# Optimization experiments

Measured on AMD Instinct MI355X. Metric: run time of the kernel, lower is better.

## Reference

```python
import jax, jax.numpy as jnp
import numpy as np

# ---- constants mirroring the torch module ----
LOSS_ALPHA = 1.0      # args.loss_weight_alpha (intra-class weight)
LOSS_BETA = 1.0       # args.loss_weight_beta (focal weight)
FOCAL_GAMMA = 2.0
FOCAL_ALPHA = 0.85
EPS = 1e-09
LDAM_S = 30.0
CLS_NUM = np.array([85.0, 900.0])
LDAM_MAX_M = 0.5
LDAM_W = np.array([0.15, 0.85], dtype=np.float32)
B = 16777216


def setup_inputs() -> dict:
    key = jax.random.key(0)
    k1, k2 = jax.random.split(key)
    x = jax.random.uniform(k1, (B, 2), dtype=jnp.float32)  # [B, 2] probabilities-like logits
    target = jax.random.randint(k2, (B,), 0, 2)            # binary labels
    return {"x": x, "target": target}


def _intraclass_p(centered, std, target, cls):
    # correlation between consecutive same-class rows (sorted-index order),
    # vectorized: class-c indices first via stable argsort, mask invalid pairs.
    n_rows = centered.shape[0]
    mask = target == cls
    n = jnp.sum(mask)
    order = jnp.argsort(jnp.where(mask, jnp.arange(n_rows), n_rows))
    a, b = order[:-1], order[1:]
    corr = jnp.sum(centered[a] * centered[b], axis=1) / (std[a] * std[b])
    valid = jnp.arange(n_rows - 1) < (n - 1)
    s = jnp.sum(jnp.where(valid, corr, 0.0))
    return jnp.where(n > 0, s / jnp.maximum(n, 1).astype(s.dtype), 0.0)


def reference(x, target):
    num_cls = x.shape[1]
    # ---- LDAM loss ----
    m = 1.0 / np.sqrt(np.sqrt(CLS_NUM))
    m = m * (LDAM_MAX_M / np.max(m))
    m_list = jnp.asarray(m, jnp.float32)
    w = jnp.asarray(LDAM_W)
    batch_m = m_list[target]                                      # [B]
    onehot = jax.nn.one_hot(target, num_cls, dtype=bool)          # [B, C]
    out = jnp.where(onehot, x - batch_m[:, None], x)              # margin on target logit only
    logsm = jax.nn.log_softmax(LDAM_S * out, axis=-1)
    nll = -jnp.take_along_axis(logsm, target[:, None], axis=1)[:, 0]
    wi = w[target]
    ldam = jnp.sum(wi * nll) / jnp.sum(wi)                        # weighted-mean cross entropy
    # ---- binary focal loss (treats x[:,1] as probability) ----
    p = x[:, 1]
    t = target.astype(x.dtype)
    fl = (-FOCAL_ALPHA * t * (1.0 - p) ** FOCAL_GAMMA * jnp.log(p + EPS)
          - (1.0 - FOCAL_ALPHA) * (1.0 - t) * p ** FOCAL_GAMMA * jnp.log(1.0 - p + EPS))
    focal = jnp.mean(fl)
    # ---- intra-class correlation loss ----
    centered = x - jnp.mean(x, axis=1, keepdims=True)
    std = jnp.std(x, axis=1, ddof=1)                               # torch.std default: unbiased
    p0 = _intraclass_p(centered, std, target, 0)
    p1 = _intraclass_p(centered, std, target, 1)
    intra = (p0 - p1) ** 2
    return ldam + LOSS_BETA * focal + LOSS_ALPHA * intra
```

## Files before the change

### kernel.cpp

```cpp
#include <hip/hip_runtime.h>

#define E_BLOCK 1024

#define M1f     0.2771814156f
#define C_A1    60.0f
#define C_C1    (30.0f*M1f - 15.0f)

#define EXP2F(v) __builtin_amdgcn_exp2f(v)
#define LOG2F(v) __builtin_amdgcn_logf(v)

__device__ __forceinline__ void comb0(int &s, int &f, int &l, int sb, int fb, int lb) {
  s += sb + l * fb;
  f = f ? f : fb;
  l = fb ? lb : l;
}

__device__ __forceinline__ void bfly_step(int m, int lane, int &s, int &f, int &l) {
  const int os = __shfl_xor(s, m), of = __shfl_xor(f, m), ol = __shfl_xor(l, m);
  const bool up = (lane & m) != 0;
  int as = up ? os : s, af = up ? of : f, al = up ? ol : l;
  const int bs = up ? s : os, bf = up ? f : of, bl = up ? l : ol;
  comb0(as, af, al, bs, bf, bl);
  s = as; f = af; l = al;
}

__device__ __forceinline__ void elem_all(float x0, float x1, int t,
    float &wnll, float &flraw, int &cnt1,
    int &s0, int &f0, int &l0, int &s1, int &f1, int &l1) {
  const float tf  = (float)t;
  const float wgt = fmaf(tf, 0.7f, 0.15f);
  const float d   = x0 - x1;
  const float za  = fmaf(tf, C_A1, -30.0f);
  const float zc  = fmaf(tf, C_C1, 15.0f);
  const float z   = fmaf(za, d, zc);
  const float ex  = EXP2F(fabsf(z) * -1.44269504f);
  const float lp  = LOG2F(1.0f + ex);
  const float sp  = fmaf(0.69314718f, lp, fmaxf(z, 0.0f));
  wnll = fmaf(wgt, sp, wnll);
  const float om  = 1.0f - x1;
  const float q   = t ? x1 : om;
  const float r   = t ? om : x1;
  const float lg2 = LOG2F(q + 1e-9f);
  const float wr2 = (wgt * r) * r;
  flraw = fmaf(wr2, lg2, flraw);
  cnt1 += t;
  const int sv = (d > 0.0f) ? 1 : -1;
  const int lv = t ? l1 : l0;
  const int add = lv * sv;
  if (t) { s1 += add; l1 = sv; f1 = f1 ? f1 : sv; }
  else   { s0 += add; l0 = sv; f0 = f0 ? f0 : sv; }
}

__global__ __launch_bounds__(256) void loss_pass1(
    const float* __restrict__ x, const int* __restrict__ tgt,
    int4* __restrict__ recs, int B) {
  __shared__ unsigned int stw[256];
  __shared__ float wnw[256];
  __shared__ float flw[256];
  __shared__ int   cnw[256];

  const int tid = threadIdx.x;
  const int w = tid >> 6, lane = tid & 63;
  const int base = blockIdx.x * E_BLOCK + tid * 4;

  float wnll = 0.f, flraw = 0.f; int cnt1 = 0;
  int s0 = 0, f0 = 0, l0 = 0, s1 = 0, f1 = 0, l1 = 0;

  if (base + 4 <= B) {
    const float4* __restrict__ px = (const float4*)(x + 2 * (size_t)base);
    const float4 a = px[0];
    const float4 b = px[1];
    const int4  t4 = *(const int4*)(tgt + base);
    elem_all(a.x, a.y, t4.x, wnll, flraw, cnt1, s0, f0, l0, s1, f1, l1);
    elem_all(a.z, a.w, t4.y, wnll, flraw, cnt1, s0, f0, l0, s1, f1, l1);
    elem_all(b.x, b.y, t4.z, wnll, flraw, cnt1, s0, f0, l0, s1, f1, l1);
    elem_all(b.z, b.w, t4.w, wnll, flraw, cnt1, s0, f0, l0, s1, f1, l1);
  } else {
    for (int k = 0; k < 4; ++k) {
      const int e = base + k;
      if (e < B) {
        elem_all(x[2 * (size_t)e], x[2 * (size_t)e + 1], tgt[e],
                 wnll, flraw, cnt1, s0, f0, l0, s1, f1, l1);
      }
    }
  }

  stw[tid] = (unsigned)(s0 + 128) | ((unsigned)(f0 + 1) << 8) | ((unsigned)(l0 + 1) << 10)
           | ((unsigned)(s1 + 128) << 16) | ((unsigned)(f1 + 1) << 24) | ((unsigned)(l1 + 1) << 26);
  wnw[tid] = wnll; flw[tid] = flraw * -0.69314718f; cnw[tid] = cnt1;
  __syncthreads();

  if (w == 0) {
    int S0 = 0, F0 = 0, L0 = 0, S1 = 0, F1 = 0, L1 = 0;
    float W = 0.f, F = 0.f; int C = 0;
    #pragma unroll
    for (int q = 0; q < 4; ++q) {
      const int i = lane * 4 + q;
      const unsigned int pk = stw[i];
      comb0(S0, F0, L0, (int)(pk & 255u) - 128, (int)((pk >> 8) & 3u) - 1, (int)((pk >> 10) & 3u) - 1);
      comb0(S1, F1, L1, (int)((pk >> 16) & 255u) - 128, (int)((pk >> 24) & 3u) - 1, (int)((pk >> 26) & 3u) - 1);
      W += wnw[i]; F += flw[i]; C += cnw[i];
    }
    #pragma unroll
    for (int k = 0; k < 6; ++k) {
      const int m = 1 << k;
      bfly_step(m, lane, S0, F0, L0);
      bfly_step(m, lane, S1, F1, L1);
      W += __shfl_xor(W, m); F += __shfl_xor(F, m); C += __shfl_xor(C, m);
    }
    if (lane == 0) {
      int4 rv;
      rv.x = (int)(((unsigned)(S0 + 1024) & 0xFFFFu) | ((unsigned)(S1 + 1024) << 16));
      rv.y = (int)((unsigned)(F0 + 1) | ((unsigned)(L0 + 1) << 2)
                 | ((unsigned)(F1 + 1) << 4) | ((unsigned)(L1 + 1) << 6)
                 | ((unsigned)C << 8));
      rv.z = __float_as_int(W);
      rv.w = __float_as_int(F);
      recs[blockIdx.x] = rv;
    }
  }
}

__global__ __launch_bounds__(256) void loss_pass2(
    const int4* __restrict__ recs, int NB, int B, float* __restrict__ out) {
  __shared__ int sS0[256], sF0[256], sL0[256], sS1[256], sF1[256], sL1[256], sC[256];
  __shared__ double sW[256], sFl[256];
  const int tid = threadIdx.x, w = tid >> 6, lane = tid & 63;
  const int R = (NB + 255) >> 8;

  int s0 = 0, f0 = 0, l0 = 0, s1 = 0, f1 = 0, l1 = 0;
  double W = 0.0, Fd = 0.0; int C = 0;
  #pragma unroll 4
  for (int r = 0; r < R; ++r) {
    const int b = tid * R + r;
    if (b < NB) {
      const int4 rv = recs[b];
      const unsigned u0 = (unsigned)rv.x, u1 = (unsigned)rv.y;
      comb0(s0, f0, l0, (int)(u0 & 0xFFFFu) - 1024, (int)(u1 & 3u) - 1, (int)((u1 >> 2) & 3u) - 1);
      comb0(s1, f1, l1, (int)(u0 >> 16) - 1024, (int)((u1 >> 4) & 3u) - 1, (int)((u1 >> 6) & 3u) - 1);
      W  += (double)__int_as_float(rv.z);
      Fd += (double)__int_as_float(rv.w);
      C  += (int)(u1 >> 8);
    }
  }
  sS0[tid] = s0; sF0[tid] = f0; sL0[tid] = l0;
  sS1[tid] = s1; sF1[tid] = f1; sL1[tid] = l1;
  sC[tid] = C; sW[tid] = W; sFl[tid] = Fd;
  __syncthreads();

  if (w == 0) {
    int S0 = 0, F0 = 0, L0 = 0, S1 = 0, F1 = 0, L1 = 0; int Ct = 0;
    double Wt = 0.0, Ft = 0.0;
    #pragma unroll
    for (int q = 0; q < 4; ++q) {
      const int i = lane * 4 + q;
      comb0(S0, F0, L0, sS0[i], sF0[i], sL0[i]);
      comb0(S1, F1, L1, sS1[i], sF1[i], sL1[i]);
      Wt += sW[i]; Ft += sFl[i]; Ct += sC[i];
    }
    #pragma unroll
    for (int k = 0; k < 6; ++k) {
      const int m = 1 << k;
      bfly_step(m, lane, S0, F0, L0);
      bfly_step(m, lane, S1, F1, L1);
      Wt += __shfl_xor(Wt, m); Ft += __shfl_xor(Ft, m); Ct += __shfl_xor(Ct, m);
    }
    if (lane == 0) {
      const double n1 = (double)Ct, n0 = (double)B - n1;
      const double sw = 0.15 * n0 + 0.85 * n1;
      const double ldam  = Wt / sw;
      const double focal = Ft / (double)B;
      const double q0 = (n0 > 0.0) ? (double)S0 / n0 : 0.0;
      const double q1 = (n1 > 0.0) ? (double)S1 / n1 : 0.0;
      const double dq = q0 - q1;
      out[0] = (float)(ldam + focal + dq * dq);
    }
  }
}

extern "C" void kernel_launch(void* const* d_in, const int* in_sizes, int n_in,
                              void* d_out, int out_size, void* d_ws, size_t ws_size,
                              hipStream_t stream) {
  const float* x  = (const float*)d_in[0];
  const int* tgt  = (const int*)d_in[1];
  float* out      = (float*)d_out;
  const int B  = in_sizes[1];
  const int NB = (B + E_BLOCK - 1) / E_BLOCK;
  int4* recs = (int4*)d_ws;
  loss_pass1<<<NB, 256, 0, stream>>>(x, tgt, recs, B);
  loss_pass2<<<1, 256, 0, stream>>>(recs, NB, B, out);
}
```

Measured before the change: 244.2 us.

## Process 16 tiles per block with double-buffered global-to-LDS async loads

Each block now handles 16 tiles of 1024 elements instead of one. Tiles are streamed through double-buffered LDS using global_load_lds, with explicit vmcnt waits so the next tile loads while the current one is computed. Per-tile sign-run partials are packed into 16-bit LDS entries and combined in order before the existing block reduction. This cuts the grid size 16x, which shrinks the pass-2 record count and per-block reduction overhead. In exchange it adds barriers per tile and leaves fewer blocks to hide memory latency.

```diff
diff --git a/kernel.cpp b/kernel.cpp
--- a/kernel.cpp
+++ b/kernel.cpp
@@ -1,6 +1,8 @@
 #include <hip/hip_runtime.h>
 
-#define E_BLOCK 1024
+#define NT 16
+#define TE 1024
+#define BLK_ELEMS (NT*TE)
 
 #define M1f     0.2771814156f
 #define C_A1    60.0f
@@ -8,6 +10,12 @@
 
 #define EXP2F(v) __builtin_amdgcn_exp2f(v)
 #define LOG2F(v) __builtin_amdgcn_logf(v)
+
+__device__ __forceinline__ void gload16(const void* g, void* l) {
+  __builtin_amdgcn_global_load_lds(
+      (const __attribute__((address_space(1))) void*)g,
+      (__attribute__((address_space(3))) void*)l, 16, 0, 0);
+}
 
 __device__ __forceinline__ void comb0(int &s, int &f, int &l, int sb, int fb, int lb) {
   s += sb + l * fb;
@@ -54,40 +62,88 @@
 __global__ __launch_bounds__(256) void loss_pass1(
     const float* __restrict__ x, const int* __restrict__ tgt,
     int4* __restrict__ recs, int B) {
+  __shared__ float4 xbuf[2][512];
+  __shared__ int4   tbuf[2][256];
+  __shared__ unsigned short seg[NT * 256];
   __shared__ unsigned int stw[256];
-  __shared__ float wnw[256];
-  __shared__ float flw[256];
+  __shared__ float wnw[256], flw[256];
   __shared__ int   cnw[256];
 
   const int tid = threadIdx.x;
   const int w = tid >> 6, lane = tid & 63;
-  const int base = blockIdx.x * E_BLOCK + tid * 4;
+  const size_t blkBase = (size_t)blockIdx.x * BLK_ELEMS;
 
   float wnll = 0.f, flraw = 0.f; int cnt1 = 0;
-  int s0 = 0, f0 = 0, l0 = 0, s1 = 0, f1 = 0, l1 = 0;
-
-  if (base + 4 <= B) {
-    const float4* __restrict__ px = (const float4*)(x + 2 * (size_t)base);
-    const float4 a = px[0];
-    const float4 b = px[1];
-    const int4  t4 = *(const int4*)(tgt + base);
-    elem_all(a.x, a.y, t4.x, wnll, flraw, cnt1, s0, f0, l0, s1, f1, l1);
-    elem_all(a.z, a.w, t4.y, wnll, flraw, cnt1, s0, f0, l0, s1, f1, l1);
-    elem_all(b.x, b.y, t4.z, wnll, flraw, cnt1, s0, f0, l0, s1, f1, l1);
-    elem_all(b.z, b.w, t4.w, wnll, flraw, cnt1, s0, f0, l0, s1, f1, l1);
+
+  if (blkBase + BLK_ELEMS <= (size_t)B) {
+    const int xg = w * 128;
+    const int tg = w * 64;
+    {
+      const float* gx = x + 2 * blkBase + (size_t)(xg + lane) * 4;
+      gload16(gx,       &xbuf[0][xg]);
+      gload16(gx + 256, &xbuf[0][xg + 64]);
+      gload16(tgt + blkBase + (size_t)(tg + lane) * 4, &tbuf[0][tg]);
+    }
+    for (int k = 0; k < NT; ++k) {
+      const int c = k & 1;
+      if (k + 1 < NT) {
+        const size_t tb = blkBase + (size_t)(k + 1) * TE;
+        const float* gx = x + 2 * tb + (size_t)(xg + lane) * 4;
+        gload16(gx,       &xbuf[c ^ 1][xg]);
+        gload16(gx + 256, &xbuf[c ^ 1][xg + 64]);
+        gload16(tgt + tb + (size_t)(tg + lane) * 4, &tbuf[c ^ 1][tg]);
+        asm volatile("s_waitcnt vmcnt(3)" ::: "memory");
+      } else {
+        asm volatile("s_waitcnt vmcnt(0)" ::: "memory");
+      }
+      __builtin_amdgcn_s_barrier();
+      __builtin_amdgcn_sched_barrier(0);
+      const float4 a  = xbuf[c][2 * tid];
+      const float4 b  = xbuf[c][2 * tid + 1];
+      const int4   t4 = tbuf[c][tid];
+      int s0 = 0, f0 = 0, l0 = 0, s1 = 0, f1 = 0, l1 = 0;
+      elem_all(a.x, a.y, t4.x, wnll, flraw, cnt1, s0, f0, l0, s1, f1, l1);
+      elem_all(a.z, a.w, t4.y, wnll, flraw, cnt1, s0, f0, l0, s1, f1, l1);
+      elem_all(b.x, b.y, t4.z, wnll, flraw, cnt1, s0, f0, l0, s1, f1, l1);
+      elem_all(b.z, b.w, t4.w, wnll, flraw, cnt1, s0, f0, l0, s1, f1, l1);
+      seg[k * 256 + tid] = (unsigned short)(
+          (unsigned)(s0 + 3) | ((unsigned)(f0 + 1) << 3) | ((unsigned)(l0 + 1) << 5) |
+          ((unsigned)(s1 + 3) << 7) | ((unsigned)(f1 + 1) << 10) | ((unsigned)(l1 + 1) << 12));
+      if (k + 1 < NT) {
+        __builtin_amdgcn_sched_barrier(0);
+        __builtin_amdgcn_s_barrier();
+        __builtin_amdgcn_sched_barrier(0);
+      }
+    }
   } else {
-    for (int k = 0; k < 4; ++k) {
-      const int e = base + k;
-      if (e < B) {
-        elem_all(x[2 * (size_t)e], x[2 * (size_t)e + 1], tgt[e],
-                 wnll, flraw, cnt1, s0, f0, l0, s1, f1, l1);
+    for (int k = 0; k < NT; ++k) {
+      int s0 = 0, f0 = 0, l0 = 0, s1 = 0, f1 = 0, l1 = 0;
+      for (int e = 0; e < 4; ++e) {
+        const size_t idx = blkBase + (size_t)k * TE + (size_t)tid * 4 + e;
+        if (idx < (size_t)B)
+          elem_all(x[2 * idx], x[2 * idx + 1], tgt[idx],
+                   wnll, flraw, cnt1, s0, f0, l0, s1, f1, l1);
       }
-    }
-  }
-
-  stw[tid] = (unsigned)(s0 + 128) | ((unsigned)(f0 + 1) << 8) | ((unsigned)(l0 + 1) << 10)
-           | ((unsigned)(s1 + 128) << 16) | ((unsigned)(f1 + 1) << 24) | ((unsigned)(l1 + 1) << 26);
-  wnw[tid] = wnll; flw[tid] = flraw * -0.69314718f; cnw[tid] = cnt1;
+      seg[k * 256 + tid] = (unsigned short)(
+          (unsigned)(s0 + 3) | ((unsigned)(f0 + 1) << 3) | ((unsigned)(l0 + 1) << 5) |
+          ((unsigned)(s1 + 3) << 7) | ((unsigned)(f1 + 1) << 10) | ((unsigned)(l1 + 1) << 12));
+    }
+  }
+  __syncthreads();
+
+  {
+    int s0 = 0, f0 = 0, l0 = 0, s1 = 0, f1 = 0, l1 = 0;
+    const int base = (tid >> 4) * 256 + (tid & 15) * 16;
+    #pragma unroll
+    for (int j = 0; j < 16; ++j) {
+      const unsigned v = seg[base + j];
+      comb0(s0, f0, l0, (int)(v & 7u) - 3, (int)((v >> 3) & 3u) - 1, (int)((v >> 5) & 3u) - 1);
+      comb0(s1, f1, l1, (int)((v >> 7) & 7u) - 3, (int)((v >> 10) & 3u) - 1, (int)((v >> 12) & 3u) - 1);
+    }
+    stw[tid] = (unsigned)(s0 + 128) | ((unsigned)(f0 + 1) << 8) | ((unsigned)(l0 + 1) << 10)
+             | ((unsigned)(s1 + 128) << 16) | ((unsigned)(f1 + 1) << 24) | ((unsigned)(l1 + 1) << 26);
+    wnw[tid] = wnll; flw[tid] = flraw * -0.69314718f; cnw[tid] = cnt1;
+  }
   __syncthreads();
 
   if (w == 0) {
@@ -110,7 +166,7 @@
     }
     if (lane == 0) {
       int4 rv;
-      rv.x = (int)(((unsigned)(S0 + 1024) & 0xFFFFu) | ((unsigned)(S1 + 1024) << 16));
+      rv.x = (int)(((unsigned)(S0 + 16384) & 0xFFFFu) | ((unsigned)(S1 + 16384) << 16));
       rv.y = (int)((unsigned)(F0 + 1) | ((unsigned)(L0 + 1) << 2)
                  | ((unsigned)(F1 + 1) << 4) | ((unsigned)(L1 + 1) << 6)
                  | ((unsigned)C << 8));
@@ -130,14 +186,13 @@
 
   int s0 = 0, f0 = 0, l0 = 0, s1 = 0, f1 = 0, l1 = 0;
   double W = 0.0, Fd = 0.0; int C = 0;
-  #pragma unroll 4
   for (int r = 0; r < R; ++r) {
     const int b = tid * R + r;
     if (b < NB) {
       const int4 rv = recs[b];
       const unsigned u0 = (unsigned)rv.x, u1 = (unsigned)rv.y;
-      comb0(s0, f0, l0, (int)(u0 & 0xFFFFu) - 1024, (int)(u1 & 3u) - 1, (int)((u1 >> 2) & 3u) - 1);
-      comb0(s1, f1, l1, (int)(u0 >> 16) - 1024, (int)((u1 >> 4) & 3u) - 1, (int)((u1 >> 6) & 3u) - 1);
+      comb0(s0, f0, l0, (int)(u0 & 0xFFFFu) - 16384, (int)(u1 & 3u) - 1, (int)((u1 >> 2) & 3u) - 1);
+      comb0(s1, f1, l1, (int)(u0 >> 16) - 16384, (int)((u1 >> 4) & 3u) - 1, (int)((u1 >> 6) & 3u) - 1);
       W  += (double)__int_as_float(rv.z);
       Fd += (double)__int_as_float(rv.w);
       C  += (int)(u1 >> 8);
@@ -185,7 +240,7 @@
   const int* tgt  = (const int*)d_in[1];
   float* out      = (float*)d_out;
   const int B  = in_sizes[1];
-  const int NB = (B + E_BLOCK - 1) / E_BLOCK;
+  const int NB = (B + BLK_ELEMS - 1) / BLK_ELEMS;
   int4* recs = (int4*)d_ws;
   loss_pass1<<<NB, 256, 0, stream>>>(x, tgt, recs, B);
   loss_pass2<<<1, 256, 0, stream>>>(recs, NB, B, out);
```

Measured after the change: 243.0 us. Within noise of the previous version (-0.5%).

## Process 8192 elements per block with wave-coalesced loads and LDS segment scan

Applied to the files above, without the earlier changes.

Each block now covers 8192 elements over 8 unrolled iterations, with wave-contiguous coalesced float4/int2 loads. Per-pair scan state goes to a padded LDS buffer and is recombined in order by a second in-block pass. This cuts the block count and the number of records the single-block second pass must reduce, which was a serial tail. The cost is extra LDS traffic, an additional barrier and more registers per thread.

```diff
diff --git a/kernel.cpp b/kernel.cpp
--- a/kernel.cpp
+++ b/kernel.cpp
@@ -1,6 +1,5 @@
 #include <hip/hip_runtime.h>
 
-#define E_BLOCK 1024
 
 #define M1f     0.2771814156f
 #define C_A1    60.0f
@@ -51,43 +50,86 @@
   else   { s0 += add; l0 = sv; f0 = f0 ? f0 : sv; }
 }
 
+__device__ __forceinline__ unsigned pack6(int s, int f, int l) {
+  return (unsigned)(s + 1) | ((unsigned)(f + 1) << 2) | ((unsigned)(l + 1) << 4);
+}
+
 __global__ __launch_bounds__(256) void loss_pass1(
     const float* __restrict__ x, const int* __restrict__ tgt,
     int4* __restrict__ recs, int B) {
+  __shared__ unsigned int segw[2176];
   __shared__ unsigned int stw[256];
-  __shared__ float wnw[256];
-  __shared__ float flw[256];
+  __shared__ float wnw[256], flw[256];
   __shared__ int   cnw[256];
 
   const int tid = threadIdx.x;
   const int w = tid >> 6, lane = tid & 63;
-  const int base = blockIdx.x * E_BLOCK + tid * 4;
+  const size_t blkBase = (size_t)blockIdx.x * 8192;
 
   float wnll = 0.f, flraw = 0.f; int cnt1 = 0;
-  int s0 = 0, f0 = 0, l0 = 0, s1 = 0, f1 = 0, l1 = 0;
-
-  if (base + 4 <= B) {
-    const float4* __restrict__ px = (const float4*)(x + 2 * (size_t)base);
-    const float4 a = px[0];
-    const float4 b = px[1];
-    const int4  t4 = *(const int4*)(tgt + base);
-    elem_all(a.x, a.y, t4.x, wnll, flraw, cnt1, s0, f0, l0, s1, f1, l1);
-    elem_all(a.z, a.w, t4.y, wnll, flraw, cnt1, s0, f0, l0, s1, f1, l1);
-    elem_all(b.x, b.y, t4.z, wnll, flraw, cnt1, s0, f0, l0, s1, f1, l1);
-    elem_all(b.z, b.w, t4.w, wnll, flraw, cnt1, s0, f0, l0, s1, f1, l1);
+
+  if (blkBase + 8192 <= (size_t)B) {
+    #pragma unroll
+    for (int it = 0; it < 8; ++it) {
+      const size_t Wb = blkBase + (size_t)it * 1024 + (size_t)w * 256;
+      const float4 xlo = *(const float4*)(x + 2 * Wb + 4 * (size_t)lane);
+      const float4 xhi = *(const float4*)(x + 2 * Wb + 256 + 4 * (size_t)lane);
+      const int2   tlo = *(const int2*)(tgt + Wb + 2 * (size_t)lane);
+      const int2   thi = *(const int2*)(tgt + Wb + 128 + 2 * (size_t)lane);
+
+      int sA0 = 0, fA0 = 0, lA0 = 0, sA1 = 0, fA1 = 0, lA1 = 0;
+      elem_all(xlo.x, xlo.y, tlo.x, wnll, flraw, cnt1, sA0, fA0, lA0, sA1, fA1, lA1);
+      elem_all(xlo.z, xlo.w, tlo.y, wnll, flraw, cnt1, sA0, fA0, lA0, sA1, fA1, lA1);
+      int sB0 = 0, fB0 = 0, lB0 = 0, sB1 = 0, fB1 = 0, lB1 = 0;
+      elem_all(xhi.x, xhi.y, thi.x, wnll, flraw, cnt1, sB0, fB0, lB0, sB1, fB1, lB1);
+      elem_all(xhi.z, xhi.w, thi.y, wnll, flraw, cnt1, sB0, fB0, lB0, sB1, fB1, lB1);
+
+      const unsigned pa = pack6(sA0, fA0, lA0) | (pack6(sA1, fA1, lA1) << 6);
+      const unsigned pb = pack6(sB0, fB0, lB0) | (pack6(sB1, fB1, lB1) << 6);
+      const int W = it * 256 + tid;
+      segw[W + (W >> 4)] = pa | (pb << 12);
+    }
   } else {
-    for (int k = 0; k < 4; ++k) {
-      const int e = base + k;
-      if (e < B) {
-        elem_all(x[2 * (size_t)e], x[2 * (size_t)e + 1], tgt[e],
-                 wnll, flraw, cnt1, s0, f0, l0, s1, f1, l1);
+    for (int it = 0; it < 8; ++it) {
+      const size_t Wb = blkBase + (size_t)it * 1024 + (size_t)w * 256;
+      int sA0 = 0, fA0 = 0, lA0 = 0, sA1 = 0, fA1 = 0, lA1 = 0;
+      int sB0 = 0, fB0 = 0, lB0 = 0, sB1 = 0, fB1 = 0, lB1 = 0;
+      for (int k = 0; k < 2; ++k) {
+        const size_t eA = Wb + 2 * (size_t)lane + k;
+        if (eA < (size_t)B)
+          elem_all(x[2 * eA], x[2 * eA + 1], tgt[eA], wnll, flraw, cnt1,
+                   sA0, fA0, lA0, sA1, fA1, lA1);
+        const size_t eB = Wb + 128 + 2 * (size_t)lane + k;
+        if (eB < (size_t)B)
+          elem_all(x[2 * eB], x[2 * eB + 1], tgt[eB], wnll, flraw, cnt1,
+                   sB0, fB0, lB0, sB1, fB1, lB1);
       }
-    }
-  }
-
-  stw[tid] = (unsigned)(s0 + 128) | ((unsigned)(f0 + 1) << 8) | ((unsigned)(l0 + 1) << 10)
-           | ((unsigned)(s1 + 128) << 16) | ((unsigned)(f1 + 1) << 24) | ((unsigned)(l1 + 1) << 26);
-  wnw[tid] = wnll; flw[tid] = flraw * -0.69314718f; cnw[tid] = cnt1;
+      const unsigned pa = pack6(sA0, fA0, lA0) | (pack6(sA1, fA1, lA1) << 6);
+      const unsigned pb = pack6(sB0, fB0, lB0) | (pack6(sB1, fB1, lB1) << 6);
+      const int W = it * 256 + tid;
+      segw[W + (W >> 4)] = pa | (pb << 12);
+    }
+  }
+  __syncthreads();
+
+  {
+    int s0 = 0, f0 = 0, l0 = 0, s1 = 0, f1 = 0, l1 = 0;
+    const int g0 = tid * 16;
+    const int it = g0 >> 9, wv = (g0 >> 7) & 3, half = (g0 >> 6) & 1;
+    const int lb = g0 & 63;
+    const int sh = half * 12;
+    const int Wbase = it * 256 + wv * 64 + lb;
+    #pragma unroll
+    for (int j = 0; j < 16; ++j) {
+      const int W = Wbase + j;
+      const unsigned v = (segw[W + (W >> 4)] >> sh) & 0xFFFu;
+      comb0(s0, f0, l0, (int)(v & 3u) - 1, (int)((v >> 2) & 3u) - 1, (int)((v >> 4) & 3u) - 1);
+      comb0(s1, f1, l1, (int)((v >> 6) & 3u) - 1, (int)((v >> 8) & 3u) - 1, (int)((v >> 10) & 3u) - 1);
+    }
+    stw[tid] = (unsigned)(s0 + 128) | ((unsigned)(f0 + 1) << 8) | ((unsigned)(l0 + 1) << 10)
+             | ((unsigned)(s1 + 128) << 16) | ((unsigned)(f1 + 1) << 24) | ((unsigned)(l1 + 1) << 26);
+    wnw[tid] = wnll; flw[tid] = flraw * -0.69314718f; cnw[tid] = cnt1;
+  }
   __syncthreads();
 
   if (w == 0) {
@@ -110,7 +152,7 @@
     }
     if (lane == 0) {
       int4 rv;
-      rv.x = (int)(((unsigned)(S0 + 1024) & 0xFFFFu) | ((unsigned)(S1 + 1024) << 16));
+      rv.x = (int)(((unsigned)(S0 + 8192) & 0xFFFFu) | ((unsigned)(S1 + 8192) << 16));
       rv.y = (int)((unsigned)(F0 + 1) | ((unsigned)(L0 + 1) << 2)
                  | ((unsigned)(F1 + 1) << 4) | ((unsigned)(L1 + 1) << 6)
                  | ((unsigned)C << 8));
@@ -130,14 +172,13 @@
 
   int s0 = 0, f0 = 0, l0 = 0, s1 = 0, f1 = 0, l1 = 0;
   double W = 0.0, Fd = 0.0; int C = 0;
-  #pragma unroll 4
   for (int r = 0; r < R; ++r) {
     const int b = tid * R + r;
     if (b < NB) {
       const int4 rv = recs[b];
       const unsigned u0 = (unsigned)rv.x, u1 = (unsigned)rv.y;
-      comb0(s0, f0, l0, (int)(u0 & 0xFFFFu) - 1024, (int)(u1 & 3u) - 1, (int)((u1 >> 2) & 3u) - 1);
-      comb0(s1, f1, l1, (int)(u0 >> 16) - 1024, (int)((u1 >> 4) & 3u) - 1, (int)((u1 >> 6) & 3u) - 1);
+      comb0(s0, f0, l0, (int)(u0 & 0xFFFFu) - 8192, (int)(u1 & 3u) - 1, (int)((u1 >> 2) & 3u) - 1);
+      comb0(s1, f1, l1, (int)(u0 >> 16) - 8192, (int)((u1 >> 4) & 3u) - 1, (int)((u1 >> 6) & 3u) - 1);
       W  += (double)__int_as_float(rv.z);
       Fd += (double)__int_as_float(rv.w);
       C  += (int)(u1 >> 8);
@@ -185,7 +226,7 @@
   const int* tgt  = (const int*)d_in[1];
   float* out      = (float*)d_out;
   const int B  = in_sizes[1];
-  const int NB = (B + E_BLOCK - 1) / E_BLOCK;
+  const int NB = (B + 8191) >> 13;
   int4* recs = (int4*)d_ws;
   loss_pass1<<<NB, 256, 0, stream>>>(x, tgt, recs, B);
   loss_pass2<<<1, 256, 0, stream>>>(recs, NB, B, out);
```

Result: no change. 240.4 us (-1.6%).

## Process four chunks per thread with inline-asm batched loads and staged waits

Applied to the files above, without the earlier changes.

Each block now covers 4096 elements instead of 1024. Every thread issues all twelve 16-byte loads up front through inline asm and consumes them in order behind explicit vmcnt waits, so memory traffic overlaps with computation. Per-chunk run-state segments are packed into shared memory and combined in a new intermediate reduction step, which also cuts the block count and the work left for pass 2. The cost is higher register pressure, hand-managed waitcnt correctness, and wider packing offsets for the larger per-block sums.

```diff
diff --git a/kernel.cpp b/kernel.cpp
--- a/kernel.cpp
+++ b/kernel.cpp
@@ -1,6 +1,8 @@
 #include <hip/hip_runtime.h>
 
-#define E_BLOCK 1024
+
+typedef float  f4 __attribute__((ext_vector_type(4)));
+typedef int    i4 __attribute__((ext_vector_type(4)));
 
 #define M1f     0.2771814156f
 #define C_A1    60.0f
@@ -53,41 +55,79 @@
 
 __global__ __launch_bounds__(256) void loss_pass1(
     const float* __restrict__ x, const int* __restrict__ tgt,
-    int4* __restrict__ recs, int B) {
+    i4* __restrict__ recs, int B) {
+  __shared__ unsigned short seg[1024];
   __shared__ unsigned int stw[256];
-  __shared__ float wnw[256];
-  __shared__ float flw[256];
+  __shared__ float wnw[256], flw[256];
   __shared__ int   cnw[256];
 
   const int tid = threadIdx.x;
   const int w = tid >> 6, lane = tid & 63;
-  const int base = blockIdx.x * E_BLOCK + tid * 4;
+  const size_t eb = (size_t)blockIdx.x * 4096;
 
   float wnll = 0.f, flraw = 0.f; int cnt1 = 0;
-  int s0 = 0, f0 = 0, l0 = 0, s1 = 0, f1 = 0, l1 = 0;
-
-  if (base + 4 <= B) {
-    const float4* __restrict__ px = (const float4*)(x + 2 * (size_t)base);
-    const float4 a = px[0];
-    const float4 b = px[1];
-    const int4  t4 = *(const int4*)(tgt + base);
-    elem_all(a.x, a.y, t4.x, wnll, flraw, cnt1, s0, f0, l0, s1, f1, l1);
-    elem_all(a.z, a.w, t4.y, wnll, flraw, cnt1, s0, f0, l0, s1, f1, l1);
-    elem_all(b.x, b.y, t4.z, wnll, flraw, cnt1, s0, f0, l0, s1, f1, l1);
-    elem_all(b.z, b.w, t4.w, wnll, flraw, cnt1, s0, f0, l0, s1, f1, l1);
+
+  if (eb + 4096 <= (size_t)B) {
+    f4 a0, a1, a2, a3, b0, b1, b2, b3;
+    i4 t0, t1, t2, t3;
+    const float* xq = x + 2 * (eb + (size_t)w * 256) + 8 * (size_t)lane;
+    const int*   tq = tgt + (eb + (size_t)w * 256) + 4 * (size_t)lane;
+    #define ISSUE(A, BV, T, OFS) \
+      asm volatile("global_load_dwordx4 %0, %1, off" : "=v"(A) : "v"(xq + 2048*(OFS))     : "memory"); \
+      asm volatile("global_load_dwordx4 %0, %1, off" : "=v"(BV) : "v"(xq + 2048*(OFS) + 4) : "memory"); \
+      asm volatile("global_load_dwordx4 %0, %1, off" : "=v"(T) : "v"(tq + 1024*(OFS))     : "memory")
+    ISSUE(a0, b0, t0, 0);
+    ISSUE(a1, b1, t1, 1);
+    ISSUE(a2, b2, t2, 2);
+    ISSUE(a3, b3, t3, 3);
+    #undef ISSUE
+
+    #define CONSUME(A, BV, T, IT, CNT) \
+      { \
+        asm volatile("s_waitcnt vmcnt(" #CNT ")" ::: "memory"); \
+        __builtin_amdgcn_sched_barrier(0); \
+        int s0 = 0, f0 = 0, l0 = 0, s1 = 0, f1 = 0, l1 = 0; \
+        elem_all(A.x, A.y, T.x, wnll, flraw, cnt1, s0, f0, l0, s1, f1, l1); \
+        elem_all(A.z, A.w, T.y, wnll, flraw, cnt1, s0, f0, l0, s1, f1, l1); \
+        elem_all(BV.x, BV.y, T.z, wnll, flraw, cnt1, s0, f0, l0, s1, f1, l1); \
+        elem_all(BV.z, BV.w, T.w, wnll, flraw, cnt1, s0, f0, l0, s1, f1, l1); \
+        seg[(IT) * 256 + w * 64 + lane] = (unsigned short)( \
+            (unsigned)(s0 + 3) | ((unsigned)(f0 + 1) << 3) | ((unsigned)(l0 + 1) << 5) | \
+            ((unsigned)(s1 + 3) << 7) | ((unsigned)(f1 + 1) << 10) | ((unsigned)(l1 + 1) << 12)); \
+      }
+    CONSUME(a0, b0, t0, 0, 9)
+    CONSUME(a1, b1, t1, 1, 6)
+    CONSUME(a2, b2, t2, 2, 3)
+    CONSUME(a3, b3, t3, 3, 0)
+    #undef CONSUME
   } else {
-    for (int k = 0; k < 4; ++k) {
-      const int e = base + k;
-      if (e < B) {
-        elem_all(x[2 * (size_t)e], x[2 * (size_t)e + 1], tgt[e],
-                 wnll, flraw, cnt1, s0, f0, l0, s1, f1, l1);
+    for (int it = 0; it < 4; ++it) {
+      int s0 = 0, f0 = 0, l0 = 0, s1 = 0, f1 = 0, l1 = 0;
+      for (int k = 0; k < 4; ++k) {
+        const size_t e = eb + (size_t)it * 1024 + (size_t)w * 256 + 4 * (size_t)lane + k;
+        if (e < (size_t)B)
+          elem_all(x[2 * e], x[2 * e + 1], tgt[e], wnll, flraw, cnt1,
+                   s0, f0, l0, s1, f1, l1);
       }
-    }
-  }
-
-  stw[tid] = (unsigned)(s0 + 128) | ((unsigned)(f0 + 1) << 8) | ((unsigned)(l0 + 1) << 10)
-           | ((unsigned)(s1 + 128) << 16) | ((unsigned)(f1 + 1) << 24) | ((unsigned)(l1 + 1) << 26);
-  wnw[tid] = wnll; flw[tid] = flraw * -0.69314718f; cnw[tid] = cnt1;
+      seg[it * 256 + w * 64 + lane] = (unsigned short)(
+          (unsigned)(s0 + 3) | ((unsigned)(f0 + 1) << 3) | ((unsigned)(l0 + 1) << 5) |
+          ((unsigned)(s1 + 3) << 7) | ((unsigned)(f1 + 1) << 10) | ((unsigned)(l1 + 1) << 12));
+    }
+  }
+  __syncthreads();
+
+  {
+    int s0 = 0, f0 = 0, l0 = 0, s1 = 0, f1 = 0, l1 = 0;
+    #pragma unroll
+    for (int j = 0; j < 4; ++j) {
+      const unsigned v = seg[tid * 4 + j];
+      comb0(s0, f0, l0, (int)(v & 7u) - 3, (int)((v >> 3) & 3u) - 1, (int)((v >> 5) & 3u) - 1);
+      comb0(s1, f1, l1, (int)((v >> 7) & 7u) - 3, (int)((v >> 10) & 3u) - 1, (int)((v >> 12) & 3u) - 1);
+    }
+    stw[tid] = (unsigned)(s0 + 128) | ((unsigned)(f0 + 1) << 8) | ((unsigned)(l0 + 1) << 10)
+             | ((unsigned)(s1 + 128) << 16) | ((unsigned)(f1 + 1) << 24) | ((unsigned)(l1 + 1) << 26);
+    wnw[tid] = wnll; flw[tid] = flraw * -0.69314718f; cnw[tid] = cnt1;
+  }
   __syncthreads();
 
   if (w == 0) {
@@ -109,8 +149,8 @@
       W += __shfl_xor(W, m); F += __shfl_xor(F, m); C += __shfl_xor(C, m);
     }
     if (lane == 0) {
-      int4 rv;
-      rv.x = (int)(((unsigned)(S0 + 1024) & 0xFFFFu) | ((unsigned)(S1 + 1024) << 16));
+      i4 rv;
+      rv.x = (int)(((unsigned)(S0 + 8192) & 0xFFFFu) | ((unsigned)(S1 + 8192) << 16));
       rv.y = (int)((unsigned)(F0 + 1) | ((unsigned)(L0 + 1) << 2)
                  | ((unsigned)(F1 + 1) << 4) | ((unsigned)(L1 + 1) << 6)
                  | ((unsigned)C << 8));
@@ -122,7 +162,7 @@
 }
 
 __global__ __launch_bounds__(256) void loss_pass2(
-    const int4* __restrict__ recs, int NB, int B, float* __restrict__ out) {
+    const i4* __restrict__ recs, int NB, int B, float* __restrict__ out) {
   __shared__ int sS0[256], sF0[256], sL0[256], sS1[256], sF1[256], sL1[256], sC[256];
   __shared__ double sW[256], sFl[256];
   const int tid = threadIdx.x, w = tid >> 6, lane = tid & 63;
@@ -130,14 +170,13 @@
 
   int s0 = 0, f0 = 0, l0 = 0, s1 = 0, f1 = 0, l1 = 0;
   double W = 0.0, Fd = 0.0; int C = 0;
-  #pragma unroll 4
   for (int r = 0; r < R; ++r) {
     const int b = tid * R + r;
     if (b < NB) {
-      const int4 rv = recs[b];
+      const i4 rv = recs[b];
       const unsigned u0 = (unsigned)rv.x, u1 = (unsigned)rv.y;
-      comb0(s0, f0, l0, (int)(u0 & 0xFFFFu) - 1024, (int)(u1 & 3u) - 1, (int)((u1 >> 2) & 3u) - 1);
-      comb0(s1, f1, l1, (int)(u0 >> 16) - 1024, (int)((u1 >> 4) & 3u) - 1, (int)((u1 >> 6) & 3u) - 1);
+      comb0(s0, f0, l0, (int)(u0 & 0xFFFFu) - 8192, (int)(u1 & 3u) - 1, (int)((u1 >> 2) & 3u) - 1);
+      comb0(s1, f1, l1, (int)(u0 >> 16) - 8192, (int)((u1 >> 4) & 3u) - 1, (int)((u1 >> 6) & 3u) - 1);
       W  += (double)__int_as_float(rv.z);
       Fd += (double)__int_as_float(rv.w);
       C  += (int)(u1 >> 8);
@@ -185,8 +224,8 @@
   const int* tgt  = (const int*)d_in[1];
   float* out      = (float*)d_out;
   const int B  = in_sizes[1];
-  const int NB = (B + E_BLOCK - 1) / E_BLOCK;
-  int4* recs = (int4*)d_ws;
+  const int NB = (B + 4095) >> 12;
+  i4* recs = (i4*)d_ws;
   loss_pass1<<<NB, 256, 0, stream>>>(x, tgt, recs, B);
   loss_pass2<<<1, 256, 0, stream>>>(recs, NB, B, out);
 }
```

New measurement: 234.8 us. -3.9%, faster.
